# Performance work log

Hardware: AMD Instinct MI355X
Metric: run time of the kernel (lower is better)

Reference implementation:

```python
import jax, jax.numpy as jnp
import numpy as np

B, H, W = 32, 56, 56
C_IN, C_OUT, GROUPS, K = 256, 256, 32, 3
EPS = 1e-5


def setup_inputs() -> dict:
    key = jax.random.key(0)
    k1, k2 = jax.random.split(key, 2)
    x = jax.random.normal(k1, (B, H, W, C_IN), dtype=jnp.float32)
    # HWIO grouped-conv kernel: I = C_IN // GROUPS = 8; equivalent to the
    # concatenation of the 32 per-group [3,3,8,8] Conv2d kernels along O.
    w = jax.random.normal(k2, (K, K, C_IN // GROUPS, C_OUT), dtype=jnp.float32) * 0.05
    b = jnp.zeros((C_OUT,), dtype=jnp.float32)
    gamma = jnp.ones((C_OUT,), dtype=jnp.float32)
    beta = jnp.zeros((C_OUT,), dtype=jnp.float32)
    return {"x": x, "w": w, "b": b, "gamma": gamma, "beta": beta}


def reference(x, w, b, gamma, beta):
    # Grouped conv: same math as tf.split -> per-group Conv2d -> tf.concat,
    # expressed as one native grouped convolution (feature_group_count).
    y = jax.lax.conv_general_dilated(
        x, w,
        window_strides=(1, 1),
        padding="SAME",
        dimension_numbers=("NHWC", "HWIO", "NHWC"),
        feature_group_count=GROUPS,
    ) + b  # [B,H,W,C_OUT]
    # BatchNorm (training forward: batch statistics over N,H,W per channel)
    mean = jnp.mean(y, axis=(0, 1, 2))
    var = jnp.var(y, axis=(0, 1, 2))
    y = (y - mean) * jax.lax.rsqrt(var + EPS) * gamma + beta
    # Act('relu')
    return jax.nn.relu(y)
```

## Files before the change

kernel.cpp:

```cpp
#include <hip/hip_runtime.h>
#include <hip/hip_bf16.h>

#define BB 32
#define HH 56
#define WW 56
#define CC 256
#define NPIX (BB*HH*WW)
#define EPS 1e-5f

typedef short bf16x8 __attribute__((ext_vector_type(8)));
typedef float f32x4  __attribute__((ext_vector_type(4)));
typedef unsigned int u32;

#define ROWB 1872

__device__ __forceinline__ unsigned short f2bf(float f) {
    __hip_bfloat16 h = __float2bfloat16(f);
    return *reinterpret_cast<unsigned short*>(&h);
}


__global__ __launch_bounds__(256, 3) void k1_conv(
    const float* __restrict__ x, const float* __restrict__ wgt,
    __hip_bfloat16* __restrict__ y, float* __restrict__ stats)
{
    __shared__ __align__(16) unsigned char xbuf[2][10*ROWB];
    __shared__ unsigned short wb[16*160];
    __shared__ float bsum[16], bsq[16];

    const int gp   = blockIdx.x;
    const int b    = blockIdx.y;
    const int hz   = blockIdx.z;
    const int t    = threadIdx.x;
    const int lane = t & 63;
    const int wv   = t >> 6;
    const int k0h  = hz*4, nb = 4 - hz;

    if (t < 16) { bsum[t] = 0.f; bsq[t] = 0.f; }

    {
        const int n  = t >> 4;
        const int kq = t & 15;
        #pragma unroll
        for (int j = 0; j < 10; ++j) {
            const int kk = kq + j*16;
            const int g  = (kk >= 80);
            const int r  = kk - g*80;
            const int tap = r >> 3, ci = r & 7;
            unsigned short val = 0;
            if (tap < 9 && (n >> 3) == g)
                val = f2bf(wgt[(tap*8 + ci)*CC + gp*16 + n]);
            wb[n*160 + kk] = val;
        }
    }

    int goff[10], soff[10];
    int mfull = 0, mfirst = 0, mlast = 0;
    #pragma unroll
    for (int j = 0; j < 10; ++j) {
        const int i   = j*256 + t;
        const int ci4 = i & 3;
        const int cq  = i >> 2;
        const int row = cq / 58;
        const int col = cq - row*58;
        goff[j] = ((row - 1)*WW + (col - 1))*CC + ci4*4;
        soff[j] = row*ROWB + col*32 + ci4*8;
        const bool ok = (i < 2320) && (col >= 1) && (col <= 56);
        if (ok) {
            mfull |= 1 << j;
            if (row != 0) mfirst |= 1 << j;
            if (row != 9) mlast  |= 1 << j;
        }
    }
    const int xbase = b*HH*WW*CC + gp*16;

    const int n    = lane & 15;
    const int q    = lane >> 4;
    const int m    = lane & 15;
    const int rowr = wv*2 + (m >> 3);
    const int colb = m & 7;
    int aoffB[5];
    #pragma unroll
    for (int s = 0; s < 5; ++s) {
        int o  = s*4 + q;
        int g  = (o >= 10);
        int tp = o - g*10;
        if (tp == 9) tp = 0;
        int dh = tp / 3, dw = tp - dh*3;
        aoffB[s] = (rowr + dh)*ROWB + (colb + dw)*32 + g*16;
    }
    const int hq = q >> 1;
    const int wq = (q & 1) * 4;

    float4 v[10];
    {
        const float* gx = x + xbase + k0h*8*WW*CC;
        const int msk = (k0h == 0) ? mfirst : mfull;
        #pragma unroll
        for (int j = 0; j < 10; ++j) {
            v[j] = make_float4(0.f, 0.f, 0.f, 0.f);
            if ((msk >> j) & 1) v[j] = *(const float4*)(gx + goff[j]);
        }
    }
    #pragma unroll
    for (int j = 0; j < 10; ++j) {
        if (j*256 + t < 2320) {
            u32 a0 = __float_as_uint(v[j].x) + 0x8000u;
            u32 a1 = __float_as_uint(v[j].y) + 0x8000u;
            u32 a2 = __float_as_uint(v[j].z) + 0x8000u;
            u32 a3 = __float_as_uint(v[j].w) + 0x8000u;
            uint2 pk;
            pk.x = __builtin_amdgcn_perm(a1, a0, 0x07060302u);
            pk.y = __builtin_amdgcn_perm(a3, a2, 0x07060302u);
            *(uint2*)(&xbuf[0][0] + soff[j]) = pk;
        }
    }
    __syncthreads();

    bf16x8 bfrag[5];
    #pragma unroll
    for (int s = 0; s < 5; ++s)
        bfrag[s] = *(const bf16x8*)(wb + n*160 + s*32 + q*8);

    float lsum = 0.f, lsq = 0.f;

    for (int kk = 0; kk < nb; ++kk) {
        const int k = k0h + kk;
        const unsigned char* cur = &xbuf[kk & 1][0];
        unsigned char* nxt = &xbuf[(kk & 1) ^ 1][0];
        const bool more = (kk + 1 < nb);

        if (more) {
            const float* gx = x + xbase + (k + 1)*8*WW*CC;
            const int msk = (k + 1 == 6) ? mlast : mfull;
            #pragma unroll
            for (int j = 0; j < 10; ++j) {
                v[j] = make_float4(0.f, 0.f, 0.f, 0.f);
                if ((msk >> j) & 1) v[j] = *(const float4*)(gx + goff[j]);
            }
        }

        #pragma unroll
        for (int ct = 0; ct < 7; ++ct) {
            f32x4 acc = {0.f, 0.f, 0.f, 0.f};
            #pragma unroll
            for (int s = 0; s < 5; ++s) {
                bf16x8 af = *(const bf16x8*)(cur + aoffB[s] + ct*256);
                acc = __builtin_amdgcn_mfma_f32_16x16x32_bf16(af, bfrag[s], acc, 0, 0, 0);
            }
            const int h = k*8 + wv*2 + hq;
            const size_t base = (((size_t)(b*HH + h))*WW + ct*8 + wq)*CC + gp*16 + n;
            #pragma unroll
            for (int i = 0; i < 4; ++i) {
                float vv = acc[i];
                y[base + (size_t)i*CC] = __float2bfloat16(vv);
                lsum += vv;
                lsq  += vv * vv;
            }
        }

        if (more) {
            #pragma unroll
            for (int j = 0; j < 10; ++j) {
                if (j*256 + t < 2320) {
                    u32 a0 = __float_as_uint(v[j].x) + 0x8000u;
                    u32 a1 = __float_as_uint(v[j].y) + 0x8000u;
                    u32 a2 = __float_as_uint(v[j].z) + 0x8000u;
                    u32 a3 = __float_as_uint(v[j].w) + 0x8000u;
                    uint2 pk;
                    pk.x = __builtin_amdgcn_perm(a1, a0, 0x07060302u);
                    pk.y = __builtin_amdgcn_perm(a3, a2, 0x07060302u);
                    *(uint2*)(nxt + soff[j]) = pk;
                }
            }
        }
        __syncthreads();
    }

    atomicAdd(&bsum[n], lsum);
    atomicAdd(&bsq[n],  lsq);
    __syncthreads();
    if (t < 16) {
        atomicAdd(&stats[gp*16 + t],       bsum[t]);
        atomicAdd(&stats[256 + gp*16 + t], bsq[t]);
    }
}

__global__ __launch_bounds__(256) void k3_norm(
    const __hip_bfloat16* __restrict__ y, const float* __restrict__ stats,
    const float* __restrict__ gamma, const float* __restrict__ beta,
    float* __restrict__ out)
{
    __shared__ float lss[512];
    const int t = threadIdx.x;
    {
        const float inv_n = 1.f / (float)NPIX;
        float mean = stats[t] * inv_n;
        float var  = stats[256 + t] * inv_n - mean * mean;
        float sc   = gamma[t] * rsqrtf(var + EPS);
        lss[t]       = sc;
        lss[256 + t] = beta[t] - mean * sc;
    }
    __syncthreads();

    const int oct = t & 31;
    const int pr  = t >> 5;
    const int c0  = oct * 8;

    float4 sc0 = *(const float4*)(lss + c0);
    float4 sc1 = *(const float4*)(lss + c0 + 4);
    float4 sh0 = *(const float4*)(lss + 256 + c0);
    float4 sh1 = *(const float4*)(lss + 256 + c0 + 4);

    const uint4* yv = (const uint4*)y;
    const int px0 = blockIdx.x * 16 + pr;

    uint4 d[2];
    #pragma unroll
    for (int i = 0; i < 2; ++i)
        d[i] = yv[(size_t)(px0 + i*8)*32 + oct];

    #pragma unroll
    for (int i = 0; i < 2; ++i) {
        const int px = px0 + i*8;
        float f0 = __uint_as_float((d[i].x & 0xffffu) << 16);
        float f1 = __uint_as_float(d[i].x & 0xffff0000u);
        float f2 = __uint_as_float((d[i].y & 0xffffu) << 16);
        float f3 = __uint_as_float(d[i].y & 0xffff0000u);
        float f4 = __uint_as_float((d[i].z & 0xffffu) << 16);
        float f5 = __uint_as_float(d[i].z & 0xffff0000u);
        float f6 = __uint_as_float((d[i].w & 0xffffu) << 16);
        float f7 = __uint_as_float(d[i].w & 0xffff0000u);

        f32x4 o0, o1;
        o0[0] = fmaxf(0.f, f0 * sc0.x + sh0.x);
        o0[1] = fmaxf(0.f, f1 * sc0.y + sh0.y);
        o0[2] = fmaxf(0.f, f2 * sc0.z + sh0.z);
        o0[3] = fmaxf(0.f, f3 * sc0.w + sh0.w);
        o1[0] = fmaxf(0.f, f4 * sc1.x + sh1.x);
        o1[1] = fmaxf(0.f, f5 * sc1.y + sh1.y);
        o1[2] = fmaxf(0.f, f6 * sc1.z + sh1.z);
        o1[3] = fmaxf(0.f, f7 * sc1.w + sh1.w);

        f32x4* op = (f32x4*)out + (size_t)px*64 + oct*2;
        __builtin_nontemporal_store(o0, op);
        __builtin_nontemporal_store(o1, op + 1);
    }
}

extern "C" void kernel_launch(void* const* d_in, const int* in_sizes, int n_in,
                              void* d_out, int out_size, void* d_ws, size_t ws_size,
                              hipStream_t stream) {
    const float* x     = (const float*)d_in[0];
    const float* wgt   = (const float*)d_in[1];
    const float* gamma = (const float*)d_in[3];
    const float* beta  = (const float*)d_in[4];
    float* out = (float*)d_out;

    float* stats = (float*)d_ws;
    __hip_bfloat16* y = (__hip_bfloat16*)((char*)d_ws + 4096);

    hipMemsetAsync(stats, 0, 2048, stream);
    k1_conv<<<dim3(16, BB, 2), 256, 0, stream>>>(x, wgt, y, stats);
    k3_norm<<<NPIX/16, 256, 0, stream>>>(y, stats, gamma, beta, out);
}
```

Before: 255.4 us.

## Retile grouped conv into spatial 4x28 tiles covering 128 channels per block

The conv kernel now tiles by spatial patch (4 rows x 28 cols plus halo) and 128 contiguous channels per block, with 8 waves each handling one 16-channel group pair. The old version used 16-channel column strips over half an image with a double-buffered row loop. The new version loads one halo tile with wide contiguous 32-byte reads per pixel, and each thread builds its weight fragments directly from global memory. The intent is better coalescing (each pixel reads 512 contiguous bytes instead of 64) and more parallel blocks. The cost is loss of load/compute overlap and redundant halo loads (6x30 rows loaded for 4x28 outputs).

```diff
diff --git a/kernel.cpp b/kernel.cpp
--- a/kernel.cpp
+++ b/kernel.cpp
@@ -12,7 +12,8 @@
 typedef float f32x4  __attribute__((ext_vector_type(4)));
 typedef unsigned int u32;
 
-#define ROWB 1872
+#define COLB 272
+#define ROWB (30*COLB)
 
 __device__ __forceinline__ unsigned short f2bf(float f) {
     __hip_bfloat16 h = __float2bfloat16(f);
@@ -20,169 +21,127 @@
 }
 
 
-__global__ __launch_bounds__(256, 3) void k1_conv(
+__global__ __launch_bounds__(512, 4) void k1_conv(
     const float* __restrict__ x, const float* __restrict__ wgt,
     __hip_bfloat16* __restrict__ y, float* __restrict__ stats)
 {
-    __shared__ __align__(16) unsigned char xbuf[2][10*ROWB];
-    __shared__ unsigned short wb[16*160];
-    __shared__ float bsum[16], bsq[16];
-
-    const int gp   = blockIdx.x;
-    const int b    = blockIdx.y;
-    const int hz   = blockIdx.z;
+    __shared__ __align__(16) unsigned char xs[6*ROWB];
+    __shared__ float bsum[128], bsq[128];
+
+    const int cq   = blockIdx.x & 1;
+    const int chh  = blockIdx.x >> 1;
+    const int hb   = blockIdx.y;
+    const int b    = blockIdx.z;
     const int t    = threadIdx.x;
     const int lane = t & 63;
-    const int wv   = t >> 6;
-    const int k0h  = hz*4, nb = 4 - hz;
-
-    if (t < 16) { bsum[t] = 0.f; bsq[t] = 0.f; }
-
-    {
-        const int n  = t >> 4;
-        const int kq = t & 15;
-        #pragma unroll
-        for (int j = 0; j < 10; ++j) {
-            const int kk = kq + j*16;
-            const int g  = (kk >= 80);
-            const int r  = kk - g*80;
-            const int tap = r >> 3, ci = r & 7;
-            unsigned short val = 0;
-            if (tap < 9 && (n >> 3) == g)
-                val = f2bf(wgt[(tap*8 + ci)*CC + gp*16 + n]);
-            wb[n*160 + kk] = val;
-        }
-    }
-
-    int goff[10], soff[10];
-    int mfull = 0, mfirst = 0, mlast = 0;
-    #pragma unroll
-    for (int j = 0; j < 10; ++j) {
-        const int i   = j*256 + t;
-        const int ci4 = i & 3;
-        const int cq  = i >> 2;
-        const int row = cq / 58;
-        const int col = cq - row*58;
-        goff[j] = ((row - 1)*WW + (col - 1))*CC + ci4*4;
-        soff[j] = row*ROWB + col*32 + ci4*8;
-        const bool ok = (i < 2320) && (col >= 1) && (col <= 56);
-        if (ok) {
-            mfull |= 1 << j;
-            if (row != 0) mfirst |= 1 << j;
-            if (row != 9) mlast  |= 1 << j;
-        }
-    }
-    const int xbase = b*HH*WW*CC + gp*16;
-
-    const int n    = lane & 15;
-    const int q    = lane >> 4;
-    const int m    = lane & 15;
-    const int rowr = wv*2 + (m >> 3);
-    const int colb = m & 7;
-    int aoffB[5];
+    const int w    = t >> 6;
+    const int r0   = hb*4, c0 = cq*28;
+    const int chbase = chh*128;
+
+    if (t < 128) { bsum[t] = 0.f; bsq[t] = 0.f; }
+
+    #pragma unroll
+    for (int jc = 0; jc < 2; ++jc) {
+        float4 a[3], c[3];
+        int so[3], iv[3];
+        #pragma unroll
+        for (int j = 0; j < 3; ++j) {
+            const int i   = (jc*3 + j)*512 + t;
+            const int oct = i & 15;
+            const int pix = i >> 4;
+            const int row = pix / 30;
+            const int col = pix - row*30;
+            const int gh  = r0 - 1 + row;
+            const int gw  = c0 - 1 + col;
+            so[j] = row*ROWB + col*COLB + oct*16;
+            iv[j] = (i < 2880);
+            const bool ok = iv[j] && ((unsigned)gh < HH) && ((unsigned)gw < WW);
+            const float* p = x + ((size_t)((b*HH + gh)*WW + gw))*CC + chbase + oct*8;
+            a[j] = ok ? *(const float4*)p       : make_float4(0.f,0.f,0.f,0.f);
+            c[j] = ok ? *(const float4*)(p + 4) : make_float4(0.f,0.f,0.f,0.f);
+        }
+        #pragma unroll
+        for (int j = 0; j < 3; ++j) {
+            if (iv[j]) {
+                u32 a0 = __float_as_uint(a[j].x) + 0x8000u;
+                u32 a1 = __float_as_uint(a[j].y) + 0x8000u;
+                u32 a2 = __float_as_uint(a[j].z) + 0x8000u;
+                u32 a3 = __float_as_uint(a[j].w) + 0x8000u;
+                u32 a4 = __float_as_uint(c[j].x) + 0x8000u;
+                u32 a5 = __float_as_uint(c[j].y) + 0x8000u;
+                u32 a6 = __float_as_uint(c[j].z) + 0x8000u;
+                u32 a7 = __float_as_uint(c[j].w) + 0x8000u;
+                uint4 pk;
+                pk.x = __builtin_amdgcn_perm(a1, a0, 0x07060302u);
+                pk.y = __builtin_amdgcn_perm(a3, a2, 0x07060302u);
+                pk.z = __builtin_amdgcn_perm(a5, a4, 0x07060302u);
+                pk.w = __builtin_amdgcn_perm(a7, a6, 0x07060302u);
+                *(uint4*)(xs + so[j]) = pk;
+            }
+        }
+    }
+
+    const int n = lane & 15;
+    const int q = lane >> 4;
+    bf16x8 bfrag[5];
     #pragma unroll
     for (int s = 0; s < 5; ++s) {
-        int o  = s*4 + q;
-        int g  = (o >= 10);
+        const int o  = s*4 + q;
+        const int g  = (o >= 10);
+        const int tp = o - g*10;
+        const int tp0 = (tp == 9) ? 0 : tp;
+        const bool val = (tp < 9) && ((n >> 3) == g);
+        const float* wp = wgt + tp0*8*CC + chbase + w*16 + n;
+        #pragma unroll
+        for (int ci = 0; ci < 8; ++ci) {
+            float f = val ? wp[ci*CC] : 0.f;
+            bfrag[s][ci] = (short)f2bf(f);
+        }
+    }
+
+    const int pr = (lane & 15) >> 2;
+    const int pc = lane & 3;
+    int aoff[5];
+    #pragma unroll
+    for (int s = 0; s < 5; ++s) {
+        const int o  = s*4 + q;
+        const int g  = (o >= 10);
         int tp = o - g*10;
         if (tp == 9) tp = 0;
-        int dh = tp / 3, dw = tp - dh*3;
-        aoffB[s] = (rowr + dh)*ROWB + (colb + dw)*32 + g*16;
-    }
-    const int hq = q >> 1;
-    const int wq = (q & 1) * 4;
-
-    float4 v[10];
-    {
-        const float* gx = x + xbase + k0h*8*WW*CC;
-        const int msk = (k0h == 0) ? mfirst : mfull;
-        #pragma unroll
-        for (int j = 0; j < 10; ++j) {
-            v[j] = make_float4(0.f, 0.f, 0.f, 0.f);
-            if ((msk >> j) & 1) v[j] = *(const float4*)(gx + goff[j]);
-        }
-    }
-    #pragma unroll
-    for (int j = 0; j < 10; ++j) {
-        if (j*256 + t < 2320) {
-            u32 a0 = __float_as_uint(v[j].x) + 0x8000u;
-            u32 a1 = __float_as_uint(v[j].y) + 0x8000u;
-            u32 a2 = __float_as_uint(v[j].z) + 0x8000u;
-            u32 a3 = __float_as_uint(v[j].w) + 0x8000u;
-            uint2 pk;
-            pk.x = __builtin_amdgcn_perm(a1, a0, 0x07060302u);
-            pk.y = __builtin_amdgcn_perm(a3, a2, 0x07060302u);
-            *(uint2*)(&xbuf[0][0] + soff[j]) = pk;
-        }
-    }
+        const int dh = tp / 3, dw = tp - dh*3;
+        aoff[s] = (pr + dh)*ROWB + (pc + dw)*COLB + (2*w + g)*16;
+    }
+
     __syncthreads();
 
-    bf16x8 bfrag[5];
-    #pragma unroll
-    for (int s = 0; s < 5; ++s)
-        bfrag[s] = *(const bf16x8*)(wb + n*160 + s*32 + q*8);
-
+    const int cb = chbase + w*16 + n;
     float lsum = 0.f, lsq = 0.f;
 
-    for (int kk = 0; kk < nb; ++kk) {
-        const int k = k0h + kk;
-        const unsigned char* cur = &xbuf[kk & 1][0];
-        unsigned char* nxt = &xbuf[(kk & 1) ^ 1][0];
-        const bool more = (kk + 1 < nb);
-
-        if (more) {
-            const float* gx = x + xbase + (k + 1)*8*WW*CC;
-            const int msk = (k + 1 == 6) ? mlast : mfull;
-            #pragma unroll
-            for (int j = 0; j < 10; ++j) {
-                v[j] = make_float4(0.f, 0.f, 0.f, 0.f);
-                if ((msk >> j) & 1) v[j] = *(const float4*)(gx + goff[j]);
-            }
-        }
-
-        #pragma unroll
-        for (int ct = 0; ct < 7; ++ct) {
-            f32x4 acc = {0.f, 0.f, 0.f, 0.f};
-            #pragma unroll
-            for (int s = 0; s < 5; ++s) {
-                bf16x8 af = *(const bf16x8*)(cur + aoffB[s] + ct*256);
-                acc = __builtin_amdgcn_mfma_f32_16x16x32_bf16(af, bfrag[s], acc, 0, 0, 0);
-            }
-            const int h = k*8 + wv*2 + hq;
-            const size_t base = (((size_t)(b*HH + h))*WW + ct*8 + wq)*CC + gp*16 + n;
-            #pragma unroll
-            for (int i = 0; i < 4; ++i) {
-                float vv = acc[i];
-                y[base + (size_t)i*CC] = __float2bfloat16(vv);
-                lsum += vv;
-                lsq  += vv * vv;
-            }
-        }
-
-        if (more) {
-            #pragma unroll
-            for (int j = 0; j < 10; ++j) {
-                if (j*256 + t < 2320) {
-                    u32 a0 = __float_as_uint(v[j].x) + 0x8000u;
-                    u32 a1 = __float_as_uint(v[j].y) + 0x8000u;
-                    u32 a2 = __float_as_uint(v[j].z) + 0x8000u;
-                    u32 a3 = __float_as_uint(v[j].w) + 0x8000u;
-                    uint2 pk;
-                    pk.x = __builtin_amdgcn_perm(a1, a0, 0x07060302u);
-                    pk.y = __builtin_amdgcn_perm(a3, a2, 0x07060302u);
-                    *(uint2*)(nxt + soff[j]) = pk;
-                }
-            }
-        }
-        __syncthreads();
-    }
-
-    atomicAdd(&bsum[n], lsum);
-    atomicAdd(&bsq[n],  lsq);
+    #pragma unroll
+    for (int ct = 0; ct < 7; ++ct) {
+        f32x4 acc = {0.f, 0.f, 0.f, 0.f};
+        #pragma unroll
+        for (int s = 0; s < 5; ++s) {
+            bf16x8 af = *(const bf16x8*)(xs + aoff[s] + ct*(4*COLB));
+            acc = __builtin_amdgcn_mfma_f32_16x16x32_bf16(af, bfrag[s], acc, 0, 0, 0);
+        }
+        const int h = r0 + q;
+        const size_t base = ((size_t)((b*HH + h)*WW + c0 + ct*4))*CC + cb;
+        #pragma unroll
+        for (int i = 0; i < 4; ++i) {
+            float vv = acc[i];
+            y[base + (size_t)i*CC] = __float2bfloat16(vv);
+            lsum += vv;
+            lsq  += vv * vv;
+        }
+    }
+
+    atomicAdd(&bsum[w*16 + n], lsum);
+    atomicAdd(&bsq[w*16 + n],  lsq);
     __syncthreads();
-    if (t < 16) {
-        atomicAdd(&stats[gp*16 + t],       bsum[t]);
-        atomicAdd(&stats[256 + gp*16 + t], bsq[t]);
+    if (t < 128) {
+        atomicAdd(&stats[chbase + t],       bsum[t]);
+        atomicAdd(&stats[256 + chbase + t], bsq[t]);
     }
 }
 
@@ -261,6 +220,6 @@
     __hip_bfloat16* y = (__hip_bfloat16*)((char*)d_ws + 4096);
 
     hipMemsetAsync(stats, 0, 2048, stream);
-    k1_conv<<<dim3(16, BB, 2), 256, 0, stream>>>(x, wgt, y, stats);
+    k1_conv<<<dim3(4, 14, BB), 512, 0, stream>>>(x, wgt, y, stats);
     k3_norm<<<NPIX/16, 256, 0, stream>>>(y, stats, gamma, beta, out);
 }
```

New measurement: 250.4 us. -2.0%, faster.
